# Kernel optimization log

Measured on AMD Instinct MI355X. Metric: run time of the kernel, lower is better.

## Reference

```python
import jax, jax.numpy as jnp
import numpy as np

C_ENC = 64
H_FEAT = 96
W_FEAT = 96
B = 2
Q = 32768
HID = 256
IN_DIM = C_ENC * 9 + 2 + 2  # 580
EPS_SHIFT = 1e-6


def _unfold3x3(feat):
    # F.unfold(feat, 3, padding=1).view(B, C*9, H, W)
    Bf, C, H, W = feat.shape
    p = jnp.pad(feat, ((0, 0), (0, 0), (1, 1), (1, 1)))
    shifts = [p[:, :, ki:ki + H, kj:kj + W] for ki in range(3) for kj in range(3)]
    return jnp.stack(shifts, axis=2).reshape(Bf, C * 9, H, W)


def _nearest_idx(g, size):
    # torch grid_sample nearest, align_corners=False: unnormalize then nearbyint
    ix = ((g + 1.0) * size - 1.0) * 0.5
    return jnp.clip(jnp.round(ix).astype(jnp.int32), 0, size - 1)


def _mlp(x, W0, b0, W1, b1, W2, b2, W3, b3, W4, b4):
    h = jax.nn.relu(x @ W0 + b0)
    h = jax.nn.relu(h @ W1 + b1)
    h = jax.nn.relu(h @ W2 + b2)
    h = jax.nn.relu(h @ W3 + b3)
    return h @ W4 + b4


def setup_inputs() -> dict:
    key = jax.random.key(0)
    ks = jax.random.split(key, 8)
    feat = jax.random.normal(ks[0], (B, C_ENC, H_FEAT, W_FEAT), jnp.float32)
    coord = jax.random.uniform(ks[1], (B, Q, 2), jnp.float32, -1.0, 1.0)
    # cell size for a ~181x181 HR grid: 2/181
    cell = jnp.full((B, Q, 2), 2.0 / 181.0, jnp.float32)
    s0 = 1.0 / np.sqrt(IN_DIM)
    sh = 1.0 / np.sqrt(HID)
    W0 = jax.random.normal(ks[2], (IN_DIM, HID), jnp.float32) * s0
    W1 = jax.random.normal(ks[3], (HID, HID), jnp.float32) * sh
    W2 = jax.random.normal(ks[4], (HID, HID), jnp.float32) * sh
    W3 = jax.random.normal(ks[5], (HID, HID), jnp.float32) * sh
    W4 = jax.random.normal(ks[6], (HID, 1), jnp.float32) * sh
    z = lambda n: jnp.zeros((n,), jnp.float32)
    return {"feat": feat, "coord": coord, "cell": cell,
            "W0": W0, "b0": z(HID), "W1": W1, "b1": z(HID),
            "W2": W2, "b2": z(HID), "W3": W3, "b3": z(HID),
            "W4": W4, "b4": z(1)}


def reference(feat, coord, cell, W0, b0, W1, b1, W2, b2, W3, b3, W4, b4):
    Bf, C, H, W = feat.shape
    feat_u = _unfold3x3(feat)                     # (B, C*9, H, W)
    feat_flat = feat_u.reshape(Bf, C * 9, H * W)  # (B, C9, HW)
    rx = 1.0 / H  # 2 / H / 2
    ry = 1.0 / W
    lo, hi = -1.0 + 1e-6, 1.0 - 1e-6
    rel_cell = cell * jnp.array([H, W], jnp.float32)  # (B,Q,2)

    preds, areas = [], []
    for vx in (-1.0, 1.0):
        for vy in (-1.0, 1.0):
            c0 = jnp.clip(coord[..., 0] + vx * rx + EPS_SHIFT, lo, hi)
            c1 = jnp.clip(coord[..., 1] + vy * ry + EPS_SHIFT, lo, hi)
            iy = _nearest_idx(c0, H)   # (B,Q) index into H dim
            ix = _nearest_idx(c1, W)
            lin = iy * W + ix
            q_feat = jnp.take_along_axis(feat_flat, lin[:, None, :], axis=2)
            q_feat = q_feat.transpose(0, 2, 1)  # (B,Q,C9)
            # pixel-center coords (= gathered make_coord grid)
            qc0 = (iy.astype(jnp.float32) + 0.5) * (2.0 / H) - 1.0
            qc1 = (ix.astype(jnp.float32) + 0.5) * (2.0 / W) - 1.0
            rel0 = (coord[..., 0] - qc0) * H
            rel1 = (coord[..., 1] - qc1) * W
            inp = jnp.concatenate(
                [q_feat, rel0[..., None], rel1[..., None], rel_cell], axis=-1)
            pred = _mlp(inp.reshape(Bf * inp.shape[1], -1),
                        W0, b0, W1, b1, W2, b2, W3, b3, W4, b4)
            preds.append(pred.reshape(Bf, -1, 1))
            areas.append(jnp.abs(rel0 * rel1) + 1e-9)

    tot_area = areas[0] + areas[1] + areas[2] + areas[3]
    # local-ensemble diagonal swap of areas
    areas = [areas[3], areas[2], areas[1], areas[0]]
    ret = jnp.zeros_like(preds[0])
    for pred, area in zip(preds, areas):
        ret = ret + pred * (area / tot_area)[..., None]
    return ret
```

## Files before the change

### kernel.cpp

```cpp
#include <hip/hip_runtime.h>
#include <hip/hip_bf16.h>

typedef __attribute__((ext_vector_type(8))) short bf16x8;
typedef __attribute__((ext_vector_type(4))) float f32x4;

__device__ inline ushort f2bf(float f) {
    union { float f; unsigned u; } x; x.f = f;
    unsigned u = x.u;
    u += 0x7fffu + ((u >> 16) & 1u);
    return (ushort)(u >> 16);
}

__device__ __forceinline__ void pack_w(const float* __restrict__ W,
                                       const float* __restrict__ bias,
                                       ushort* __restrict__ Wp,
                                       int idx, int NKT, int Nstride, int mode) {
    int lane = idx & 63;
    int kt = (idx >> 6) % NKT;
    int nt = idx / (64 * NKT);
    int n = nt * 16 + (lane & 15);
    int kbase = kt * 32 + (lane >> 4) * 8;
    ushort o[8];
    #pragma unroll
    for (int i = 0; i < 8; ++i) {
        int k = kbase + i;
        float v = 0.0f;
        if (mode == 0) {
            if (k < 576) { int tap = k >> 6, c = k & 63; v = W[(c * 9 + tap) * Nstride + n]; }
            else if (k < 580) v = W[k * Nstride + n];
            else if (k == 580) v = bias[n];
        } else if (mode == 1) {
            v = W[k * Nstride + n];
        } else {
            v = (n == 0) ? W[k] : 0.0f;
        }
        o[i] = f2bf(v);
    }
    *reinterpret_cast<uint4*>(Wp + (size_t)idx * 8) = *reinterpret_cast<const uint4*>(o);
}

__global__ void prep_all_k(const float* __restrict__ feat,
                           const float* __restrict__ W0, const float* __restrict__ W1,
                           const float* __restrict__ W2, const float* __restrict__ W3,
                           const float* __restrict__ W4, const float* __restrict__ b0,
                           ushort* __restrict__ featT,
                           ushort* __restrict__ W0p, ushort* __restrict__ W1p,
                           ushort* __restrict__ W2p, ushort* __restrict__ W3p,
                           ushort* __restrict__ W4p) {
    int bid = blockIdx.x;
    if (bid < 4802) {
        int idx = bid * 256 + threadIdx.x;
        if (idx >= 2 * 98 * 98 * 64) return;
        int c = idx & 63;
        int rest = idx >> 6;
        int x = rest % 98; rest /= 98;
        int y = rest % 98;
        int b = rest / 98;
        ushort v = 0;
        if (x >= 1 && x <= 96 && y >= 1 && y <= 96)
            v = f2bf(feat[((b * 64 + c) * 96 + (y - 1)) * 96 + (x - 1)]);
        featT[idx] = v;
    } else if (bid < 4878) {
        int idx = (bid - 4802) * 256 + threadIdx.x;
        if (idx < 16 * 19 * 64) pack_w(W0, b0, W0p, idx, 19, 256, 0);
    } else if (bid < 4910) {
        int idx = (bid - 4878) * 256 + threadIdx.x;
        if (idx < 16 * 8 * 64) pack_w(W1, b0, W1p, idx, 8, 256, 1);
    } else if (bid < 4942) {
        int idx = (bid - 4910) * 256 + threadIdx.x;
        if (idx < 16 * 8 * 64) pack_w(W2, b0, W2p, idx, 8, 256, 1);
    } else if (bid < 4974) {
        int idx = (bid - 4942) * 256 + threadIdx.x;
        if (idx < 16 * 8 * 64) pack_w(W3, b0, W3p, idx, 8, 256, 1);
    } else {
        int idx = (bid - 4974) * 256 + threadIdx.x;
        if (idx < 1 * 8 * 64) pack_w(W4, b0, W4p, idx, 8, 1, 2);
    }
}

__device__ __forceinline__ int SW(int p) { return p ^ ((p >> 4) & 3); }

__global__ __launch_bounds__(256, 3) void liif_main(
    const float* __restrict__ coord, const float* __restrict__ cell,
    const ushort* __restrict__ featT,
    const ushort* __restrict__ W0p, const ushort* __restrict__ W1p,
    const ushort* __restrict__ W2p, const ushort* __restrict__ W3p,
    const ushort* __restrict__ W4p,
    const float* __restrict__ b1, const float* __restrict__ b2,
    const float* __restrict__ b3, const float* __restrict__ b4,
    float* __restrict__ out)
{
    __shared__ ushort buf[4 * 8 * 64 * 8];
    __shared__ float pred_lds[64];
    __shared__ float area_lds[64];

    const int t = threadIdx.x;
    const int lane = t & 63;
    const int w = t >> 6;
    const int g = lane >> 4;
    const int l15 = lane & 15;
    const int swl = SW(lane);

    const ushort* p0;
    ushort* g_lds;
    uint ex01, ex23, ex45;
    {
        const int r = t >> 2, sub = t & 3;
        const int qi = r >> 2, s = r & 3;
        const int gq = blockIdx.x * 16 + qi;
        const int bidx = gq >> 15;
        const float vx = (s & 2) ? 1.0f : -1.0f;
        const float vy = (s & 1) ? 1.0f : -1.0f;
        const float rxf = (float)(1.0 / 96.0);
        const float lo = (float)(-1.0 + 1e-6);
        const float hi = (float)(1.0 - 1e-6);
        float c0 = coord[gq * 2 + 0], c1 = coord[gq * 2 + 1];
        float cl0 = cell[gq * 2 + 0], cl1 = cell[gq * 2 + 1];
        float sc0 = fminf(fmaxf(__fadd_rn(__fadd_rn(c0, vx * rxf), 1e-6f), lo), hi);
        float sc1 = fminf(fmaxf(__fadd_rn(__fadd_rn(c1, vy * rxf), 1e-6f), lo), hi);
        float fy = __fmul_rn(__fadd_rn(__fmul_rn(__fadd_rn(sc0, 1.0f), 96.0f), -1.0f), 0.5f);
        float fx = __fmul_rn(__fadd_rn(__fmul_rn(__fadd_rn(sc1, 1.0f), 96.0f), -1.0f), 0.5f);
        int iy = (int)rintf(fy); iy = iy < 0 ? 0 : (iy > 95 ? 95 : iy);
        int ix = (int)rintf(fx); ix = ix < 0 ? 0 : (ix > 95 ? 95 : ix);
        float qc0 = (iy + 0.5f) * (float)(2.0 / 96.0) - 1.0f;
        float qc1 = (ix + 0.5f) * (float)(2.0 / 96.0) - 1.0f;
        float rel0 = (c0 - qc0) * 96.0f;
        float rel1 = (c1 - qc1) * 96.0f;
        if (sub == 0) {
            area_lds[r] = fabsf(rel0 * rel1) + 1e-9f;
            asm("v_cvt_pk_bf16_f32 %0, %1, %2" : "=v"(ex01) : "v"(rel0), "v"(rel1));
            float rc0 = cl0 * 96.0f, rc1 = cl1 * 96.0f;
            asm("v_cvt_pk_bf16_f32 %0, %1, %2" : "=v"(ex23) : "v"(rc0), "v"(rc1));
            ex45 = 0x3F80u;
        } else {
            ex01 = 0; ex23 = 0; ex45 = 0;
        }
        const int g_rt = r >> 4;
        const int g_sw = SW((r & 15) + (sub << 4));
        p0 = featT + (size_t)bidx * 98 * 98 * 64 + (iy * 98 + ix) * 64 + sub * 8;
        g_lds = buf + (g_rt * 8 * 64 + g_sw) * 8;
    }

    const int hi8 = l15 >> 3;
    ushort* sp  = buf + w * 1024 + g * 32 + hi8 * 128 + (l15 & 7);
    ushort* spE = sp + 8 * hi8;
    ushort* spO = sp - 8 * hi8;

    f32x4 acc[4][4];

    auto store_acts = [&]() {
        #pragma unroll
        for (int ct = 0; ct < 4; ++ct)
            #pragma unroll
            for (int rt = 0; rt < 4; ++rt) {
                float v0 = fmaxf(acc[rt][ct][0], 0.0f);
                float v1 = fmaxf(acc[rt][ct][1], 0.0f);
                float v2 = fmaxf(acc[rt][ct][2], 0.0f);
                float v3 = fmaxf(acc[rt][ct][3], 0.0f);
                uint p01, p23;
                asm("v_cvt_pk_bf16_f32 %0, %1, %2" : "=v"(p01) : "v"(v0), "v"(v1));
                asm("v_cvt_pk_bf16_f32 %0, %1, %2" : "=v"(p23) : "v"(v2), "v"(v3));
                const int off = rt * 4096 + (ct >> 1) * 512 + (ct & 1) * 256;
                if ((ct & 1) == 0) {
                    spE[off + 0]  = (ushort)p01;
                    spO[off + 8]  = (ushort)(p01 >> 16);
                    spE[off + 16] = (ushort)p23;
                    spO[off + 24] = (ushort)(p23 >> 16);
                } else {
                    spE[off + 16] = (ushort)p01;
                    spO[off + 24] = (ushort)(p01 >> 16);
                    spE[off + 0]  = (ushort)p23;
                    spO[off + 8]  = (ushort)(p23 >> 16);
                }
            }
    };

#define LOADW0(DST, KT) do { _Pragma("unroll")                                   \
        for (int ct_ = 0; ct_ < 4; ++ct_)                                        \
            DST[ct_] = *reinterpret_cast<const bf16x8*>(                         \
                W0p + (((size_t)(w * 4 + ct_) * 19 + (KT)) * 64 + lane) * 8);    \
    } while (0)
#define LOADWX(DST, WP, KT) do { _Pragma("unroll")                               \
        for (int ct_ = 0; ct_ < 4; ++ct_)                                        \
            DST[ct_] = *reinterpret_cast<const bf16x8*>(                         \
                (WP) + (((size_t)(w * 4 + ct_) * 8 + (KT)) * 64 + lane) * 8);    \
    } while (0)
#define MFMA_LINE(BFR, LINE) do { _Pragma("unroll")                              \
        for (int rt_ = 0; rt_ < 4; ++rt_) {                                      \
            bf16x8 a_ = *reinterpret_cast<const bf16x8*>(                        \
                buf + ((rt_ * 8 + (LINE)) * 64 + swl) * 8);                      \
            _Pragma("unroll")                                                    \
            for (int ct_ = 0; ct_ < 4; ++ct_)                                    \
                acc[rt_][ct_] = __builtin_amdgcn_mfma_f32_16x16x32_bf16(         \
                    a_, BFR[ct_], acc[rt_][ct_], 0, 0, 0);                       \
        } } while (0)
#define MFMA_LINE_C(BFR, LINE, BC) do { _Pragma("unroll")                        \
        for (int rt_ = 0; rt_ < 4; ++rt_) {                                      \
            bf16x8 a_ = *reinterpret_cast<const bf16x8*>(                        \
                buf + ((rt_ * 8 + (LINE)) * 64 + swl) * 8);                      \
            _Pragma("unroll")                                                    \
            for (int ct_ = 0; ct_ < 4; ++ct_)                                    \
                acc[rt_][ct_] = __builtin_amdgcn_mfma_f32_16x16x32_bf16(         \
                    a_, BFR[ct_], (BC)[ct_], 0, 0, 0);                           \
        } } while (0)
#define G1(KT, LINE) do {                                                        \
        constexpr int tap_ = (KT) >> 1;                                          \
        constexpr int coff_ = ((tap_ / 3) * 98 + (tap_ % 3)) * 64 + ((KT) & 1) * 32; \
        *reinterpret_cast<uint4*>(g_lds + (LINE) * 512) =                        \
            *reinterpret_cast<const uint4*>(p0 + coff_);                         \
    } while (0)

    bf16x8 wA[4], wB[4];
    f32x4 zc[4];
    #pragma unroll
    for (int c_ = 0; c_ < 4; ++c_) { zc[c_][0] = 0.f; zc[c_][1] = 0.f; zc[c_][2] = 0.f; zc[c_][3] = 0.f; }
    G1(0, 0); G1(1, 1); G1(2, 2); G1(3, 3); G1(4, 4); G1(5, 5); G1(6, 6); G1(7, 7);
    LOADW0(wA, 0); LOADW0(wB, 1);
    __syncthreads();
    __builtin_amdgcn_s_setprio(1);
    MFMA_LINE_C(wA, 0, zc); LOADW0(wA, 2);
    MFMA_LINE(wB, 1);       LOADW0(wB, 3);
    #pragma unroll 1
    for (int i = 2; i < 8; i += 2) {
        MFMA_LINE(wA, i);     LOADW0(wA, i + 2);
        MFMA_LINE(wB, i + 1); LOADW0(wB, i + 3);
    }
    __builtin_amdgcn_s_setprio(0);
    __syncthreads();
    G1(8, 0); G1(9, 1); G1(10, 2); G1(11, 3); G1(12, 4); G1(13, 5); G1(14, 6); G1(15, 7);
    __syncthreads();
    __builtin_amdgcn_s_setprio(1);
    #pragma unroll 1
    for (int i = 0; i < 8; i += 2) {
        MFMA_LINE(wA, i);     LOADW0(wA, i + 10);
        MFMA_LINE(wB, i + 1); LOADW0(wB, i + 11);
    }
    __builtin_amdgcn_s_setprio(0);
    __syncthreads();
    G1(16, 0); G1(17, 1);
    *reinterpret_cast<uint4*>(g_lds + 2 * 512) = make_uint4(ex01, ex23, ex45, 0);
    __syncthreads();
    __builtin_amdgcn_s_setprio(1);
    MFMA_LINE(wA, 0); LOADW0(wA, 18);
    MFMA_LINE(wB, 1);
    MFMA_LINE(wA, 2);
    __builtin_amdgcn_s_setprio(0);
    __syncthreads();

    #pragma unroll 1
    for (int layer = 0; layer < 3; ++layer) {
        store_acts();
        const ushort* Wp = (layer == 0) ? W1p : (layer == 1) ? W2p : W3p;
        const float* bias = (layer == 0) ? b1 : (layer == 1) ? b2 : b3;
        f32x4 bc[4];
        #pragma unroll
        for (int ct = 0; ct < 4; ++ct) {
            float bv = bias[(w * 4 + ct) * 16 + l15];
            bc[ct][0] = bv; bc[ct][1] = bv; bc[ct][2] = bv; bc[ct][3] = bv;
        }
        const int k0 = 2 * w;
        LOADWX(wA, Wp, k0);
        __builtin_amdgcn_s_setprio(1);
        LOADWX(wB, Wp, k0 + 1);
        MFMA_LINE_C(wA, k0, bc); LOADWX(wA, Wp, (k0 + 2) & 7);
        MFMA_LINE(wB, k0 + 1);   LOADWX(wB, Wp, (k0 + 3) & 7);
        __builtin_amdgcn_s_setprio(0);
        __syncthreads();
        __builtin_amdgcn_s_setprio(1);
        MFMA_LINE(wA, (k0 + 2) & 7); LOADWX(wA, Wp, (k0 + 4) & 7);
        MFMA_LINE(wB, (k0 + 3) & 7); LOADWX(wB, Wp, (k0 + 5) & 7);
        MFMA_LINE(wA, (k0 + 4) & 7); LOADWX(wA, Wp, (k0 + 6) & 7);
        MFMA_LINE(wB, (k0 + 5) & 7); LOADWX(wB, Wp, (k0 + 7) & 7);
        MFMA_LINE(wA, (k0 + 6) & 7);
        MFMA_LINE(wB, (k0 + 7) & 7);
        __builtin_amdgcn_s_setprio(0);
        __syncthreads();
    }
    store_acts();
    __syncthreads();

    {
        float b4v = b4[0];
        f32x4 a5;
        a5[0] = b4v; a5[1] = b4v; a5[2] = b4v; a5[3] = b4v;
        #pragma unroll
        for (int kt = 0; kt < 8; ++kt) {
            bf16x8 bb = *reinterpret_cast<const bf16x8*>(W4p + ((size_t)kt * 64 + lane) * 8);
            bf16x8 aa = *reinterpret_cast<const bf16x8*>(buf + ((w * 8 + kt) * 64 + swl) * 8);
            a5 = __builtin_amdgcn_mfma_f32_16x16x32_bf16(aa, bb, a5, 0, 0, 0);
        }
        if (l15 == 0) {
            #pragma unroll
            for (int j = 0; j < 4; ++j)
                pred_lds[w * 16 + (g << 2) + j] = a5[j];
        }
    }
    __syncthreads();

    if (t < 16) {
        int oq = blockIdx.x * 16 + t;
        float p0v = pred_lds[t * 4 + 0], p1v = pred_lds[t * 4 + 1];
        float p2v = pred_lds[t * 4 + 2], p3v = pred_lds[t * 4 + 3];
        float a0 = area_lds[t * 4 + 0], a1 = area_lds[t * 4 + 1];
        float a2 = area_lds[t * 4 + 2], a3 = area_lds[t * 4 + 3];
        float tot = a0 + a1 + a2 + a3;
        out[oq] = (p0v * a3 + p1v * a2 + p2v * a1 + p3v * a0) / tot;
    }
#undef G1
#undef LOADW0
#undef LOADWX
#undef MFMA_LINE
#undef MFMA_LINE_C
}

extern "C" void kernel_launch(void* const* d_in, const int* in_sizes, int n_in,
                              void* d_out, int out_size, void* d_ws, size_t ws_size,
                              hipStream_t stream) {
    const float* feat  = (const float*)d_in[0];
    const float* coord = (const float*)d_in[1];
    const float* cell  = (const float*)d_in[2];
    const float* W0 = (const float*)d_in[3];
    const float* b0 = (const float*)d_in[4];
    const float* W1 = (const float*)d_in[5];
    const float* b1 = (const float*)d_in[6];
    const float* W2 = (const float*)d_in[7];
    const float* b2 = (const float*)d_in[8];
    const float* W3 = (const float*)d_in[9];
    const float* b3 = (const float*)d_in[10];
    const float* W4 = (const float*)d_in[11];
    const float* b4 = (const float*)d_in[12];
    float* out = (float*)d_out;

    ushort* featT = (ushort*)d_ws;
    ushort* W0p = featT + 1229312;
    ushort* W1p = W0p + 155648;
    ushort* W2p = W1p + 65536;
    ushort* W3p = W2p + 65536;
    ushort* W4p = W3p + 65536;

    prep_all_k<<<4976, 256, 0, stream>>>(feat, W0, W1, W2, W3, W4, b0,
                                         featT, W0p, W1p, W2p, W3p, W4p);
    liif_main<<<4096, 256, 0, stream>>>(coord, cell, featT, W0p, W1p, W2p, W3p, W4p,
                                        b1, b2, b3, b4, out);
}
```

Measured before the change: 176.3 us.

## Split MLP output columns across eight waves per block instead of four

Doubles the block size to 512 threads so each wave computes two 16-column tiles instead of four. The feature gather is split between thread pairs and the hidden-layer weight-load rotation is restaged. The goal is more waves in flight and fewer accumulator registers per wave, to hide MFMA and load latency. In exchange, every A-fragment read from LDS is now shared by fewer MFMAs, and each block has more barrier participants.

```diff
diff --git a/kernel.cpp b/kernel.cpp
--- a/kernel.cpp
+++ b/kernel.cpp
@@ -80,7 +80,7 @@
 
 __device__ __forceinline__ int SW(int p) { return p ^ ((p >> 4) & 3); }
 
-__global__ __launch_bounds__(256, 3) void liif_main(
+__global__ __launch_bounds__(512, 6) void liif_main(
     const float* __restrict__ coord, const float* __restrict__ cell,
     const ushort* __restrict__ featT,
     const ushort* __restrict__ W0p, const ushort* __restrict__ W1p,
@@ -104,8 +104,11 @@
     const ushort* p0;
     ushort* g_lds;
     uint ex01, ex23, ex45;
+    int ps;
     {
-        const int r = t >> 2, sub = t & 3;
+        const int r = t >> 3, sub8 = t & 7;
+        const int sub = sub8 & 3;
+        ps = sub8 >> 2;
         const int qi = r >> 2, s = r & 3;
         const int gq = blockIdx.x * 16 + qi;
         const int bidx = gq >> 15;
@@ -126,7 +129,7 @@
         float qc1 = (ix + 0.5f) * (float)(2.0 / 96.0) - 1.0f;
         float rel0 = (c0 - qc0) * 96.0f;
         float rel1 = (c1 - qc1) * 96.0f;
-        if (sub == 0) {
+        if (sub8 == 0) {
             area_lds[r] = fabsf(rel0 * rel1) + 1e-9f;
             asm("v_cvt_pk_bf16_f32 %0, %1, %2" : "=v"(ex01) : "v"(rel0), "v"(rel1));
             float rc0 = cl0 * 96.0f, rc1 = cl1 * 96.0f;
@@ -142,26 +145,26 @@
     }
 
     const int hi8 = l15 >> 3;
-    ushort* sp  = buf + w * 1024 + g * 32 + hi8 * 128 + (l15 & 7);
+    ushort* sp  = buf + w * 512 + g * 32 + hi8 * 128 + (l15 & 7);
     ushort* spE = sp + 8 * hi8;
     ushort* spO = sp - 8 * hi8;
 
-    f32x4 acc[4][4];
+    f32x4 acc[4][2];
 
     auto store_acts = [&]() {
         #pragma unroll
-        for (int ct = 0; ct < 4; ++ct)
+        for (int cc = 0; cc < 2; ++cc)
             #pragma unroll
             for (int rt = 0; rt < 4; ++rt) {
-                float v0 = fmaxf(acc[rt][ct][0], 0.0f);
-                float v1 = fmaxf(acc[rt][ct][1], 0.0f);
-                float v2 = fmaxf(acc[rt][ct][2], 0.0f);
-                float v3 = fmaxf(acc[rt][ct][3], 0.0f);
+                float v0 = fmaxf(acc[rt][cc][0], 0.0f);
+                float v1 = fmaxf(acc[rt][cc][1], 0.0f);
+                float v2 = fmaxf(acc[rt][cc][2], 0.0f);
+                float v3 = fmaxf(acc[rt][cc][3], 0.0f);
                 uint p01, p23;
                 asm("v_cvt_pk_bf16_f32 %0, %1, %2" : "=v"(p01) : "v"(v0), "v"(v1));
                 asm("v_cvt_pk_bf16_f32 %0, %1, %2" : "=v"(p23) : "v"(v2), "v"(v3));
-                const int off = rt * 4096 + (ct >> 1) * 512 + (ct & 1) * 256;
-                if ((ct & 1) == 0) {
+                const int off = rt * 4096 + cc * 256;
+                if (cc == 0) {
                     spE[off + 0]  = (ushort)p01;
                     spO[off + 8]  = (ushort)(p01 >> 16);
                     spE[off + 16] = (ushort)p23;
@@ -176,32 +179,32 @@
     };
 
 #define LOADW0(DST, KT) do { _Pragma("unroll")                                   \
-        for (int ct_ = 0; ct_ < 4; ++ct_)                                        \
-            DST[ct_] = *reinterpret_cast<const bf16x8*>(                         \
-                W0p + (((size_t)(w * 4 + ct_) * 19 + (KT)) * 64 + lane) * 8);    \
+        for (int cc_ = 0; cc_ < 2; ++cc_)                                        \
+            DST[cc_] = *reinterpret_cast<const bf16x8*>(                         \
+                W0p + (((size_t)(w * 2 + cc_) * 19 + (KT)) * 64 + lane) * 8);    \
     } while (0)
 #define LOADWX(DST, WP, KT) do { _Pragma("unroll")                               \
-        for (int ct_ = 0; ct_ < 4; ++ct_)                                        \
-            DST[ct_] = *reinterpret_cast<const bf16x8*>(                         \
-                (WP) + (((size_t)(w * 4 + ct_) * 8 + (KT)) * 64 + lane) * 8);    \
+        for (int cc_ = 0; cc_ < 2; ++cc_)                                        \
+            DST[cc_] = *reinterpret_cast<const bf16x8*>(                         \
+                (WP) + (((size_t)(w * 2 + cc_) * 8 + (KT)) * 64 + lane) * 8);    \
     } while (0)
 #define MFMA_LINE(BFR, LINE) do { _Pragma("unroll")                              \
         for (int rt_ = 0; rt_ < 4; ++rt_) {                                      \
             bf16x8 a_ = *reinterpret_cast<const bf16x8*>(                        \
                 buf + ((rt_ * 8 + (LINE)) * 64 + swl) * 8);                      \
             _Pragma("unroll")                                                    \
-            for (int ct_ = 0; ct_ < 4; ++ct_)                                    \
-                acc[rt_][ct_] = __builtin_amdgcn_mfma_f32_16x16x32_bf16(         \
-                    a_, BFR[ct_], acc[rt_][ct_], 0, 0, 0);                       \
+            for (int cc_ = 0; cc_ < 2; ++cc_)                                    \
+                acc[rt_][cc_] = __builtin_amdgcn_mfma_f32_16x16x32_bf16(         \
+                    a_, BFR[cc_], acc[rt_][cc_], 0, 0, 0);                       \
         } } while (0)
 #define MFMA_LINE_C(BFR, LINE, BC) do { _Pragma("unroll")                        \
         for (int rt_ = 0; rt_ < 4; ++rt_) {                                      \
             bf16x8 a_ = *reinterpret_cast<const bf16x8*>(                        \
                 buf + ((rt_ * 8 + (LINE)) * 64 + swl) * 8);                      \
             _Pragma("unroll")                                                    \
-            for (int ct_ = 0; ct_ < 4; ++ct_)                                    \
-                acc[rt_][ct_] = __builtin_amdgcn_mfma_f32_16x16x32_bf16(         \
-                    a_, BFR[ct_], (BC)[ct_], 0, 0, 0);                           \
+            for (int cc_ = 0; cc_ < 2; ++cc_)                                    \
+                acc[rt_][cc_] = __builtin_amdgcn_mfma_f32_16x16x32_bf16(         \
+                    a_, BFR[cc_], (BC)[cc_], 0, 0, 0);                           \
         } } while (0)
 #define G1(KT, LINE) do {                                                        \
         constexpr int tap_ = (KT) >> 1;                                          \
@@ -210,11 +213,12 @@
             *reinterpret_cast<const uint4*>(p0 + coff_);                         \
     } while (0)
 
-    bf16x8 wA[4], wB[4];
-    f32x4 zc[4];
+    bf16x8 wA[2], wB[2];
+    f32x4 zc[2];
     #pragma unroll
-    for (int c_ = 0; c_ < 4; ++c_) { zc[c_][0] = 0.f; zc[c_][1] = 0.f; zc[c_][2] = 0.f; zc[c_][3] = 0.f; }
-    G1(0, 0); G1(1, 1); G1(2, 2); G1(3, 3); G1(4, 4); G1(5, 5); G1(6, 6); G1(7, 7);
+    for (int c_ = 0; c_ < 2; ++c_) { zc[c_][0] = 0.f; zc[c_][1] = 0.f; zc[c_][2] = 0.f; zc[c_][3] = 0.f; }
+    if (ps == 0) { G1(0, 0); G1(2, 2); G1(4, 4); G1(6, 6); }
+    else         { G1(1, 1); G1(3, 3); G1(5, 5); G1(7, 7); }
     LOADW0(wA, 0); LOADW0(wB, 1);
     __syncthreads();
     __builtin_amdgcn_s_setprio(1);
@@ -227,7 +231,8 @@
     }
     __builtin_amdgcn_s_setprio(0);
     __syncthreads();
-    G1(8, 0); G1(9, 1); G1(10, 2); G1(11, 3); G1(12, 4); G1(13, 5); G1(14, 6); G1(15, 7);
+    if (ps == 0) { G1(8, 0); G1(10, 2); G1(12, 4); G1(14, 6); }
+    else         { G1(9, 1); G1(11, 3); G1(13, 5); G1(15, 7); }
     __syncthreads();
     __builtin_amdgcn_s_setprio(1);
     #pragma unroll 1
@@ -237,8 +242,12 @@
     }
     __builtin_amdgcn_s_setprio(0);
     __syncthreads();
-    G1(16, 0); G1(17, 1);
-    *reinterpret_cast<uint4*>(g_lds + 2 * 512) = make_uint4(ex01, ex23, ex45, 0);
+    if (ps == 0) {
+        G1(16, 0);
+        *reinterpret_cast<uint4*>(g_lds + 2 * 512) = make_uint4(ex01, ex23, ex45, 0);
+    } else {
+        G1(17, 1);
+    }
     __syncthreads();
     __builtin_amdgcn_s_setprio(1);
     MFMA_LINE(wA, 0); LOADW0(wA, 18);
@@ -249,37 +258,36 @@
 
     #pragma unroll 1
     for (int layer = 0; layer < 3; ++layer) {
-        store_acts();
         const ushort* Wp = (layer == 0) ? W1p : (layer == 1) ? W2p : W3p;
         const float* bias = (layer == 0) ? b1 : (layer == 1) ? b2 : b3;
-        f32x4 bc[4];
+        LOADWX(wA, Wp, w);
+        store_acts();
+        f32x4 bc[2];
         #pragma unroll
-        for (int ct = 0; ct < 4; ++ct) {
-            float bv = bias[(w * 4 + ct) * 16 + l15];
-            bc[ct][0] = bv; bc[ct][1] = bv; bc[ct][2] = bv; bc[ct][3] = bv;
-        }
-        const int k0 = 2 * w;
-        LOADWX(wA, Wp, k0);
+        for (int cc = 0; cc < 2; ++cc) {
+            float bv = bias[(w * 2 + cc) * 16 + l15];
+            bc[cc][0] = bv; bc[cc][1] = bv; bc[cc][2] = bv; bc[cc][3] = bv;
+        }
         __builtin_amdgcn_s_setprio(1);
-        LOADWX(wB, Wp, k0 + 1);
-        MFMA_LINE_C(wA, k0, bc); LOADWX(wA, Wp, (k0 + 2) & 7);
-        MFMA_LINE(wB, k0 + 1);   LOADWX(wB, Wp, (k0 + 3) & 7);
+        LOADWX(wB, Wp, (w + 1) & 7);
+        MFMA_LINE_C(wA, w, bc); LOADWX(wA, Wp, (w + 2) & 7);
         __builtin_amdgcn_s_setprio(0);
         __syncthreads();
         __builtin_amdgcn_s_setprio(1);
-        MFMA_LINE(wA, (k0 + 2) & 7); LOADWX(wA, Wp, (k0 + 4) & 7);
-        MFMA_LINE(wB, (k0 + 3) & 7); LOADWX(wB, Wp, (k0 + 5) & 7);
-        MFMA_LINE(wA, (k0 + 4) & 7); LOADWX(wA, Wp, (k0 + 6) & 7);
-        MFMA_LINE(wB, (k0 + 5) & 7); LOADWX(wB, Wp, (k0 + 7) & 7);
-        MFMA_LINE(wA, (k0 + 6) & 7);
-        MFMA_LINE(wB, (k0 + 7) & 7);
+        MFMA_LINE(wB, (w + 1) & 7); LOADWX(wB, Wp, (w + 3) & 7);
+        MFMA_LINE(wA, (w + 2) & 7); LOADWX(wA, Wp, (w + 4) & 7);
+        MFMA_LINE(wB, (w + 3) & 7); LOADWX(wB, Wp, (w + 5) & 7);
+        MFMA_LINE(wA, (w + 4) & 7); LOADWX(wA, Wp, (w + 6) & 7);
+        MFMA_LINE(wB, (w + 5) & 7); LOADWX(wB, Wp, (w + 7) & 7);
+        MFMA_LINE(wA, (w + 6) & 7);
+        MFMA_LINE(wB, (w + 7) & 7);
         __builtin_amdgcn_s_setprio(0);
         __syncthreads();
     }
     store_acts();
     __syncthreads();
 
-    {
+    if (w < 4) {
         float b4v = b4[0];
         f32x4 a5;
         a5[0] = b4v; a5[1] = b4v; a5[2] = b4v; a5[3] = b4v;
@@ -340,6 +348,6 @@
 
     prep_all_k<<<4976, 256, 0, stream>>>(feat, W0, W1, W2, W3, W4, b0,
                                          featT, W0p, W1p, W2p, W3p, W4p);
-    liif_main<<<4096, 256, 0, stream>>>(coord, cell, featT, W0p, W1p, W2p, W3p, W4p,
+    liif_main<<<4096, 512, 0, stream>>>(coord, cell, featT, W0p, W1p, W2p, W3p, W4p,
                                         b1, b2, b3, b4, out);
 }
```

Measured after the change: 228.4 us. 1.3x slower.

## Use direct global-to-LDS loads and double-buffer layer-0 feature gathers

Applied to the files above, without the earlier changes.

Replaces the register-staged gather of unfolded feature rows with global_load_lds direct-to-LDS transfers, remapping threads so each wave fills its own LDS lines. The layer-0 K loop is restructured into half-buffer stages, so the next gather is issued while MFMAs consume the other half, removing separate gather/sync phases. The first weight-fragment load of each hidden layer is also hoisted ahead of the activation store. This relies on the async LDS write ordering and the new row-to-lane mapping matching the swizzled layout the MFMA reads expect.

```diff
diff --git a/kernel.cpp b/kernel.cpp
--- a/kernel.cpp
+++ b/kernel.cpp
@@ -102,11 +102,12 @@
     const int swl = SW(lane);
 
     const ushort* p0;
-    ushort* g_lds;
-    uint ex01, ex23, ex45;
+    uint exA, exB, exC;
     {
-        const int r = t >> 2, sub = t & 3;
-        const int qi = r >> 2, s = r & 3;
+        const int chunk = lane >> 4;
+        const int row16 = l15 ^ ((lane >> 4) & 3);
+        const int row = 16 * w + row16;
+        const int qi = row >> 2, s = row & 3;
         const int gq = blockIdx.x * 16 + qi;
         const int bidx = gq >> 15;
         const float vx = (s & 2) ? 1.0f : -1.0f;
@@ -126,19 +127,16 @@
         float qc1 = (ix + 0.5f) * (float)(2.0 / 96.0) - 1.0f;
         float rel0 = (c0 - qc0) * 96.0f;
         float rel1 = (c1 - qc1) * 96.0f;
-        if (sub == 0) {
-            area_lds[r] = fabsf(rel0 * rel1) + 1e-9f;
-            asm("v_cvt_pk_bf16_f32 %0, %1, %2" : "=v"(ex01) : "v"(rel0), "v"(rel1));
+        if (chunk == 0) {
+            area_lds[row] = fabsf(rel0 * rel1) + 1e-9f;
+            asm("v_cvt_pk_bf16_f32 %0, %1, %2" : "=v"(exA) : "v"(rel0), "v"(rel1));
             float rc0 = cl0 * 96.0f, rc1 = cl1 * 96.0f;
-            asm("v_cvt_pk_bf16_f32 %0, %1, %2" : "=v"(ex23) : "v"(rc0), "v"(rc1));
-            ex45 = 0x3F80u;
+            asm("v_cvt_pk_bf16_f32 %0, %1, %2" : "=v"(exB) : "v"(rc0), "v"(rc1));
+            exC = 0x3F80u;
         } else {
-            ex01 = 0; ex23 = 0; ex45 = 0;
-        }
-        const int g_rt = r >> 4;
-        const int g_sw = SW((r & 15) + (sub << 4));
-        p0 = featT + (size_t)bidx * 98 * 98 * 64 + (iy * 98 + ix) * 64 + sub * 8;
-        g_lds = buf + (g_rt * 8 * 64 + g_sw) * 8;
+            exA = 0; exB = 0; exC = 0;
+        }
+        p0 = featT + (size_t)bidx * 98 * 98 * 64 + (iy * 98 + ix) * 64 + chunk * 8;
     }
 
     const int hi8 = l15 >> 3;
@@ -203,42 +201,54 @@
                 acc[rt_][ct_] = __builtin_amdgcn_mfma_f32_16x16x32_bf16(         \
                     a_, BFR[ct_], (BC)[ct_], 0, 0, 0);                           \
         } } while (0)
-#define G1(KT, LINE) do {                                                        \
+#define GLDS(KT, LINE) do {                                                      \
         constexpr int tap_ = (KT) >> 1;                                          \
         constexpr int coff_ = ((tap_ / 3) * 98 + (tap_ % 3)) * 64 + ((KT) & 1) * 32; \
-        *reinterpret_cast<uint4*>(g_lds + (LINE) * 512) =                        \
-            *reinterpret_cast<const uint4*>(p0 + coff_);                         \
+        __builtin_amdgcn_global_load_lds(                                        \
+            (const __attribute__((address_space(1))) void*)(p0 + coff_),         \
+            (__attribute__((address_space(3))) void*)(buf + (w * 8 + (LINE)) * 512), \
+            16, 0, 0);                                                           \
     } while (0)
 
     bf16x8 wA[4], wB[4];
     f32x4 zc[4];
     #pragma unroll
     for (int c_ = 0; c_ < 4; ++c_) { zc[c_][0] = 0.f; zc[c_][1] = 0.f; zc[c_][2] = 0.f; zc[c_][3] = 0.f; }
-    G1(0, 0); G1(1, 1); G1(2, 2); G1(3, 3); G1(4, 4); G1(5, 5); G1(6, 6); G1(7, 7);
+    GLDS(0, 0); GLDS(1, 1); GLDS(2, 2); GLDS(3, 3);
     LOADW0(wA, 0); LOADW0(wB, 1);
     __syncthreads();
+    GLDS(4, 4); GLDS(5, 5); GLDS(6, 6); GLDS(7, 7);
     __builtin_amdgcn_s_setprio(1);
     MFMA_LINE_C(wA, 0, zc); LOADW0(wA, 2);
     MFMA_LINE(wB, 1);       LOADW0(wB, 3);
-    #pragma unroll 1
-    for (int i = 2; i < 8; i += 2) {
-        MFMA_LINE(wA, i);     LOADW0(wA, i + 2);
-        MFMA_LINE(wB, i + 1); LOADW0(wB, i + 3);
-    }
-    __builtin_amdgcn_s_setprio(0);
-    __syncthreads();
-    G1(8, 0); G1(9, 1); G1(10, 2); G1(11, 3); G1(12, 4); G1(13, 5); G1(14, 6); G1(15, 7);
-    __syncthreads();
-    __builtin_amdgcn_s_setprio(1);
-    #pragma unroll 1
-    for (int i = 0; i < 8; i += 2) {
-        MFMA_LINE(wA, i);     LOADW0(wA, i + 10);
-        MFMA_LINE(wB, i + 1); LOADW0(wB, i + 11);
-    }
-    __builtin_amdgcn_s_setprio(0);
-    __syncthreads();
-    G1(16, 0); G1(17, 1);
-    *reinterpret_cast<uint4*>(g_lds + 2 * 512) = make_uint4(ex01, ex23, ex45, 0);
+    MFMA_LINE(wA, 2);       LOADW0(wA, 4);
+    MFMA_LINE(wB, 3);       LOADW0(wB, 5);
+    __builtin_amdgcn_s_setprio(0);
+    __syncthreads();
+    GLDS(8, 0); GLDS(9, 1); GLDS(10, 2); GLDS(11, 3);
+    __builtin_amdgcn_s_setprio(1);
+    MFMA_LINE(wA, 4); LOADW0(wA, 6);
+    MFMA_LINE(wB, 5); LOADW0(wB, 7);
+    MFMA_LINE(wA, 6); LOADW0(wA, 8);
+    MFMA_LINE(wB, 7); LOADW0(wB, 9);
+    __builtin_amdgcn_s_setprio(0);
+    __syncthreads();
+    GLDS(12, 4); GLDS(13, 5); GLDS(14, 6); GLDS(15, 7);
+    __builtin_amdgcn_s_setprio(1);
+    MFMA_LINE(wA, 0); LOADW0(wA, 10);
+    MFMA_LINE(wB, 1); LOADW0(wB, 11);
+    MFMA_LINE(wA, 2); LOADW0(wA, 12);
+    MFMA_LINE(wB, 3); LOADW0(wB, 13);
+    __builtin_amdgcn_s_setprio(0);
+    __syncthreads();
+    GLDS(16, 0); GLDS(17, 1);
+    *reinterpret_cast<uint4*>(&buf[((w * 8 + 2) * 64 + lane) * 8]) = make_uint4(exA, exB, exC, 0);
+    __builtin_amdgcn_s_setprio(1);
+    MFMA_LINE(wA, 4); LOADW0(wA, 14);
+    MFMA_LINE(wB, 5); LOADW0(wB, 15);
+    MFMA_LINE(wA, 6); LOADW0(wA, 16);
+    MFMA_LINE(wB, 7); LOADW0(wB, 17);
+    __builtin_amdgcn_s_setprio(0);
     __syncthreads();
     __builtin_amdgcn_s_setprio(1);
     MFMA_LINE(wA, 0); LOADW0(wA, 18);
@@ -249,17 +259,17 @@
 
     #pragma unroll 1
     for (int layer = 0; layer < 3; ++layer) {
-        store_acts();
         const ushort* Wp = (layer == 0) ? W1p : (layer == 1) ? W2p : W3p;
         const float* bias = (layer == 0) ? b1 : (layer == 1) ? b2 : b3;
+        const int k0 = 2 * w;
+        LOADWX(wA, Wp, k0);
+        store_acts();
         f32x4 bc[4];
         #pragma unroll
         for (int ct = 0; ct < 4; ++ct) {
             float bv = bias[(w * 4 + ct) * 16 + l15];
             bc[ct][0] = bv; bc[ct][1] = bv; bc[ct][2] = bv; bc[ct][3] = bv;
         }
-        const int k0 = 2 * w;
-        LOADWX(wA, Wp, k0);
         __builtin_amdgcn_s_setprio(1);
         LOADWX(wB, Wp, k0 + 1);
         MFMA_LINE_C(wA, k0, bc); LOADWX(wA, Wp, (k0 + 2) & 7);
@@ -306,7 +316,7 @@
         float tot = a0 + a1 + a2 + a3;
         out[oq] = (p0v * a3 + p1v * a2 + p2v * a1 + p3v * a0) / tot;
     }
-#undef G1
+#undef GLDS
 #undef LOADW0
 #undef LOADWX
 #undef MFMA_LINE
```

After: 182.8 us. 1.04x slower.
